# Kernel optimization log

Hardware: AMD Instinct MI355X
Metric: run time of the kernel (lower is better)

The kernel has to match this reference:

```python
import jax, jax.numpy as jnp
from jax import lax
import numpy as np

B, T, H, P = 256, 2048, 256, 24

def setup_inputs() -> dict:
    key = jax.random.key(0)
    ks = jax.random.split(key, 7)
    s_ih = 1.0 / np.sqrt(H)
    return {
        "x": jax.random.normal(ks[0], (B, T, 1), dtype=jnp.float32),
        "W_ih": jax.random.normal(ks[1], (H, 1), dtype=jnp.float32) * s_ih,
        "W_hh": jax.random.normal(ks[2], (H, H), dtype=jnp.float32) * s_ih,
        "b_ih": jax.random.normal(ks[3], (H,), dtype=jnp.float32) * s_ih,
        "b_hh": jax.random.normal(ks[4], (H,), dtype=jnp.float32) * s_ih,
        "W_out": jax.random.normal(ks[5], (P, H), dtype=jnp.float32) * s_ih,
        "b_out": jax.random.normal(ks[6], (P,), dtype=jnp.float32) * s_ih,
    }

def reference(x, W_ih, W_hh, b_ih, b_hh, W_out, b_out):
    # Precompute input projection for all timesteps: [B,T,H]
    xp = jnp.einsum('bti,hi->bth', x, W_ih) + b_ih + b_hh
    h0 = jnp.zeros((x.shape[0], W_hh.shape[0]), dtype=x.dtype)

    def step(h, xt):  # xt: [B,H]
        h_new = jnp.tanh(xt + h @ W_hh.T)
        return h_new, None

    hT, _ = lax.scan(step, h0, xp.transpose(1, 0, 2))  # scan over T
    # Linear head on last hidden state: [B,P]
    return hT @ W_out.T + b_out
```

## Files before the change

### kernel.cpp

```cpp
#include <hip/hip_runtime.h>


#define BB 256
#define TT 2048
#define HH 256
#define PP 24
#define HSTR 20

typedef float v2f __attribute__((ext_vector_type(2)));

struct alignas(16) hquad { v2f lo, hi; };

__device__ __forceinline__ int hidx(int k) { return (k >> 4) * HSTR + (k & 15); }

template<int CTRL>
__device__ __forceinline__ float dppadd(float dst, float src) {
    return dst + __int_as_float(__builtin_amdgcn_update_dpp(
        0, __float_as_int(src), CTRL, 0xf, 0xf, true));
}

__device__ __forceinline__ void lds_barrier() {
    asm volatile("s_waitcnt lgkmcnt(0)\n\ts_barrier" ::: "memory");
}

__global__ __launch_bounds__(512, 1)
void rnn_persist(const float* __restrict__ x,
                 const float* __restrict__ W_ih,
                 const float* __restrict__ W_hh,
                 const float* __restrict__ b_ih,
                 const float* __restrict__ b_hh,
                 const float* __restrict__ W_out,
                 const float* __restrict__ b_out,
                 float* __restrict__ out)
{
    __shared__ __align__(16) float hbuf[2][16 * HSTR];

    const int tid = threadIdx.x;
    const int b   = blockIdx.x;
    const int c   = tid & 15;
    const int g   = tid >> 4;

    hbuf[0][hidx(tid & 255)] = 0.0f;

    const int m[8] = {0, 2, 7, 5, 8, 10, 15, 13};

    v2f w2[8][8];
    #pragma unroll
    for (int s = 0; s < 8; ++s) {
        const int row_idx = 8 * g + ((c ^ m[s]) >> 1);
        const float* row = W_hh + row_idx * HH + 16 * c;
        #pragma unroll
        for (int j = 0; j < 4; ++j) {
            const float4 q = *(const float4*)(row + 4 * j);
            w2[s][2 * j + 0] = (v2f){q.x, q.y};
            w2[s][2 * j + 1] = (v2f){q.z, q.w};
        }
    }

    const int   o_fin = 8 * g + (c >> 1);
    const float wih   = W_ih[o_fin];
    const float cb    = b_ih[o_fin] + b_hh[o_fin];
    const int   widx  = hidx(o_fin);

    __syncthreads();

    const float* hc0 = hbuf[0] + c * HSTR;
    const float* hc1 = hbuf[1] + c * HSTR;
    const float* xb  = x + b * TT;

    auto step = [&](const float* __restrict__ cur, float* __restrict__ nxt,
                    float xt) __attribute__((always_inline)) {
        const hquad* hq = (const hquad*)cur;
        const hquad q0 = hq[0], q1 = hq[1], q2 = hq[2], q3 = hq[3];

        v2f acc[8];
        #pragma unroll
        for (int s = 0; s < 8; ++s) acc[s] = w2[s][0] * q0.lo;
        #pragma unroll
        for (int s = 0; s < 8; ++s)
            acc[s] = __builtin_elementwise_fma(w2[s][1], q0.hi, acc[s]);
        #pragma unroll
        for (int s = 0; s < 8; ++s)
            acc[s] = __builtin_elementwise_fma(w2[s][2], q1.lo, acc[s]);
        #pragma unroll
        for (int s = 0; s < 8; ++s)
            acc[s] = __builtin_elementwise_fma(w2[s][3], q1.hi, acc[s]);
        #pragma unroll
        for (int s = 0; s < 8; ++s)
            acc[s] = __builtin_elementwise_fma(w2[s][4], q2.lo, acc[s]);
        #pragma unroll
        for (int s = 0; s < 8; ++s)
            acc[s] = __builtin_elementwise_fma(w2[s][5], q2.hi, acc[s]);
        #pragma unroll
        for (int s = 0; s < 8; ++s)
            acc[s] = __builtin_elementwise_fma(w2[s][6], q3.lo, acc[s]);
        #pragma unroll
        for (int s = 0; s < 8; ++s)
            acc[s] = __builtin_elementwise_fma(w2[s][7], q3.hi, acc[s]);

        float aa[8];
        #pragma unroll
        for (int s = 0; s < 8; ++s) aa[s] = acc[s].x + acc[s].y;

        float b0 = dppadd<0x128>(aa[0], aa[4]);
        float b1 = dppadd<0x128>(aa[1], aa[5]);
        float b2 = dppadd<0x128>(aa[2], aa[6]);
        float b3 = dppadd<0x128>(aa[3], aa[7]);
        float c0 = dppadd<0x141>(b0, b2);
        float c1 = dppadd<0x141>(b1, b3);
        float d  = dppadd<0x4E>(c0, c1);
        float e  = dppadd<0xB1>(d, d);

        const float u  = fmaf(xt, wih, cb) + e;
        const float p  = __builtin_amdgcn_exp2f(u * 2.8853900817779268f);
        const float th = fmaf(-2.f, __builtin_amdgcn_rcpf(p + 1.f), 1.f);
        nxt[widx] = th;
        lds_barrier();
    };

    float4 xa = *(const float4*)(xb + 0);
    float4 xc = *(const float4*)(xb + 4);
    for (int t = 0; t < TT; t += 8) {
        const int tn = (t + 8 < TT) ? (t + 8) : t;
        const float4 xa_n = *(const float4*)(xb + tn);
        const float4 xc_n = *(const float4*)(xb + tn + 4);
        step(hc0, hbuf[1], xa.x);
        step(hc1, hbuf[0], xa.y);
        step(hc0, hbuf[1], xa.z);
        step(hc1, hbuf[0], xa.w);
        step(hc0, hbuf[1], xc.x);
        step(hc1, hbuf[0], xc.y);
        step(hc0, hbuf[1], xc.z);
        step(hc1, hbuf[0], xc.w);
        xa = xa_n;
        xc = xc_n;
    }

    if (tid < PP) {
        const float* wo = W_out + tid * HH;
        float s0 = 0.f, s1 = 0.f, s2 = 0.f, s3 = 0.f;
        #pragma unroll
        for (int h = 0; h < HH; h += 4) {
            s0 = fmaf(wo[h + 0], hbuf[0][hidx(h + 0)], s0);
            s1 = fmaf(wo[h + 1], hbuf[0][hidx(h + 1)], s1);
            s2 = fmaf(wo[h + 2], hbuf[0][hidx(h + 2)], s2);
            s3 = fmaf(wo[h + 3], hbuf[0][hidx(h + 3)], s3);
        }
        out[b * PP + tid] = b_out[tid] + (s0 + s1) + (s2 + s3);
    }
}

extern "C" void kernel_launch(void* const* d_in, const int* in_sizes, int n_in,
                              void* d_out, int out_size, void* d_ws, size_t ws_size,
                              hipStream_t stream) {
    const float* x     = (const float*)d_in[0];
    const float* W_ih  = (const float*)d_in[1];
    const float* W_hh  = (const float*)d_in[2];
    const float* b_ih  = (const float*)d_in[3];
    const float* b_hh  = (const float*)d_in[4];
    const float* W_out = (const float*)d_in[5];
    const float* b_out = (const float*)d_in[6];
    float* out = (float*)d_out;

    rnn_persist<<<BB, 512, 0, stream>>>(x, W_ih, W_hh, b_ih, b_hh, W_out, b_out, out);
}
```

Measured before the change: 967.8 us.

## Halve block to 256 threads, each computing a full output with 256 weights

Each block now uses 256 threads instead of 512. Every thread owns one hidden unit, holds 256 W_hh weights in registers instead of 128, and does twice the FMAs per step using scalar FMAs rather than packed v2f FMAs. The DPP reduction changes from a fold of pair sums into a 16-way butterfly. This cuts barrier participants and wave count per block. In exchange it doubles per-thread arithmetic and register pressure, with a risk of spilling and of losing packed-FMA throughput.

```diff
diff --git a/kernel.cpp b/kernel.cpp
--- a/kernel.cpp
+++ b/kernel.cpp
@@ -6,10 +6,6 @@
 #define HH 256
 #define PP 24
 #define HSTR 20
-
-typedef float v2f __attribute__((ext_vector_type(2)));
-
-struct alignas(16) hquad { v2f lo, hi; };
 
 __device__ __forceinline__ int hidx(int k) { return (k >> 4) * HSTR + (k & 15); }
 
@@ -23,7 +19,7 @@
     asm volatile("s_waitcnt lgkmcnt(0)\n\ts_barrier" ::: "memory");
 }
 
-__global__ __launch_bounds__(512, 1)
+__global__ __launch_bounds__(256, 1)
 void rnn_persist(const float* __restrict__ x,
                  const float* __restrict__ W_ih,
                  const float* __restrict__ W_hh,
@@ -40,24 +36,24 @@
     const int c   = tid & 15;
     const int g   = tid >> 4;
 
-    hbuf[0][hidx(tid & 255)] = 0.0f;
+    hbuf[0][hidx(tid)] = 0.0f;
 
-    const int m[8] = {0, 2, 7, 5, 8, 10, 15, 13};
+    const int m16[16] = {0,1,2,3, 7,6,5,4, 8,9,10,11, 15,14,13,12};
 
-    v2f w2[8][8];
+    float w[16][16];
     #pragma unroll
-    for (int s = 0; s < 8; ++s) {
-        const int row_idx = 8 * g + ((c ^ m[s]) >> 1);
+    for (int s = 0; s < 16; ++s) {
+        const int row_idx = 16 * g + (c ^ m16[s]);
         const float* row = W_hh + row_idx * HH + 16 * c;
         #pragma unroll
         for (int j = 0; j < 4; ++j) {
-            const float4 q = *(const float4*)(row + 4 * j);
-            w2[s][2 * j + 0] = (v2f){q.x, q.y};
-            w2[s][2 * j + 1] = (v2f){q.z, q.w};
+            const float4 qv = *(const float4*)(row + 4 * j);
+            w[s][4*j+0] = qv.x; w[s][4*j+1] = qv.y;
+            w[s][4*j+2] = qv.z; w[s][4*j+3] = qv.w;
         }
     }
 
-    const int   o_fin = 8 * g + (c >> 1);
+    const int   o_fin = 16 * g + c;
     const float wih   = W_ih[o_fin];
     const float cb    = b_ih[o_fin] + b_hh[o_fin];
     const int   widx  = hidx(o_fin);
@@ -70,46 +66,40 @@
 
     auto step = [&](const float* __restrict__ cur, float* __restrict__ nxt,
                     float xt) __attribute__((always_inline)) {
-        const hquad* hq = (const hquad*)cur;
-        const hquad q0 = hq[0], q1 = hq[1], q2 = hq[2], q3 = hq[3];
+        const float4* hq = (const float4*)cur;
+        const float4 Q0 = hq[0], Q1 = hq[1], Q2 = hq[2], Q3 = hq[3];
+        const float q[16] = {Q0.x,Q0.y,Q0.z,Q0.w, Q1.x,Q1.y,Q1.z,Q1.w,
+                             Q2.x,Q2.y,Q2.z,Q2.w, Q3.x,Q3.y,Q3.z,Q3.w};
 
-        v2f acc[8];
+        float ae[16], ao[16];
         #pragma unroll
-        for (int s = 0; s < 8; ++s) acc[s] = w2[s][0] * q0.lo;
+        for (int s = 0; s < 16; ++s) ae[s] = w[s][0] * q[0];
         #pragma unroll
-        for (int s = 0; s < 8; ++s)
-            acc[s] = __builtin_elementwise_fma(w2[s][1], q0.hi, acc[s]);
+        for (int s = 0; s < 16; ++s) ao[s] = w[s][1] * q[1];
         #pragma unroll
-        for (int s = 0; s < 8; ++s)
-            acc[s] = __builtin_elementwise_fma(w2[s][2], q1.lo, acc[s]);
+        for (int jj = 1; jj < 8; ++jj) {
+            #pragma unroll
+            for (int s = 0; s < 16; ++s)
+                ae[s] = fmaf(w[s][2*jj], q[2*jj], ae[s]);
+            #pragma unroll
+            for (int s = 0; s < 16; ++s)
+                ao[s] = fmaf(w[s][2*jj+1], q[2*jj+1], ao[s]);
+        }
+
+        float aa[16];
         #pragma unroll
-        for (int s = 0; s < 8; ++s)
-            acc[s] = __builtin_elementwise_fma(w2[s][3], q1.hi, acc[s]);
+        for (int s = 0; s < 16; ++s) aa[s] = ae[s] + ao[s];
+
+        float t8[8];
         #pragma unroll
-        for (int s = 0; s < 8; ++s)
-            acc[s] = __builtin_elementwise_fma(w2[s][4], q2.lo, acc[s]);
+        for (int s = 0; s < 8; ++s) t8[s] = dppadd<0x128>(aa[s], aa[s+8]);
+        float t4[4];
         #pragma unroll
-        for (int s = 0; s < 8; ++s)
-            acc[s] = __builtin_elementwise_fma(w2[s][5], q2.hi, acc[s]);
-        #pragma unroll
-        for (int s = 0; s < 8; ++s)
-            acc[s] = __builtin_elementwise_fma(w2[s][6], q3.lo, acc[s]);
-        #pragma unroll
-        for (int s = 0; s < 8; ++s)
-            acc[s] = __builtin_elementwise_fma(w2[s][7], q3.hi, acc[s]);
-
-        float aa[8];
-        #pragma unroll
-        for (int s = 0; s < 8; ++s) aa[s] = acc[s].x + acc[s].y;
-
-        float b0 = dppadd<0x128>(aa[0], aa[4]);
-        float b1 = dppadd<0x128>(aa[1], aa[5]);
-        float b2 = dppadd<0x128>(aa[2], aa[6]);
-        float b3 = dppadd<0x128>(aa[3], aa[7]);
-        float c0 = dppadd<0x141>(b0, b2);
-        float c1 = dppadd<0x141>(b1, b3);
-        float d  = dppadd<0x4E>(c0, c1);
-        float e  = dppadd<0xB1>(d, d);
+        for (int s = 0; s < 4; ++s) t4[s] = dppadd<0x141>(t8[s], t8[s+4]);
+        float t2[2];
+        t2[0] = dppadd<0x4E>(t4[0], t4[2]);
+        t2[1] = dppadd<0x4E>(t4[1], t4[3]);
+        const float e = dppadd<0xB1>(t2[0], t2[1]);
 
         const float u  = fmaf(xt, wih, cb) + e;
         const float p  = __builtin_amdgcn_exp2f(u * 2.8853900817779268f);
@@ -162,5 +152,5 @@
     const float* b_out = (const float*)d_in[6];
     float* out = (float*)d_out;
 
-    rnn_persist<<<BB, 512, 0, stream>>>(x, W_ih, W_hh, b_ih, b_hh, W_out, b_out, out);
+    rnn_persist<<<BB, 256, 0, stream>>>(x, W_ih, W_hh, b_ih, b_hh, W_out, b_out, out);
 }
```

Result: slower. 3.693 ms (+281.6%).

## Store hidden state and recurrent weights in fp16 and use packed dot2

Applied to the files above, without the earlier changes.

Converts the register-resident W_hh slice and the LDS hidden-state buffer to fp16 and replaces packed fp32 FMAs with v_dot2 fp16-to-fp32 accumulation. This halves the instruction count of the per-step matvec and halves LDS read traffic (two 16-byte loads instead of four), and it removes the final pairwise add of accumulator halves. The cost is reduced precision: the hidden state is rounded to fp16 every step across 2048 recurrent steps, which may exceed the accuracy tolerance.

```diff
diff --git a/kernel.cpp b/kernel.cpp
--- a/kernel.cpp
+++ b/kernel.cpp
@@ -5,18 +5,27 @@
 #define TT 2048
 #define HH 256
 #define PP 24
-#define HSTR 20
+#define HSTRH 24
 
-typedef float v2f __attribute__((ext_vector_type(2)));
+typedef _Float16 half_t;
+typedef _Float16 h2 __attribute__((ext_vector_type(2)));
 
-struct alignas(16) hquad { v2f lo, hi; };
+struct alignas(16) hoct { h2 v[4]; };
 
-__device__ __forceinline__ int hidx(int k) { return (k >> 4) * HSTR + (k & 15); }
+__device__ __forceinline__ int hidx16(int k) { return (k >> 4) * HSTRH + (k & 15); }
 
 template<int CTRL>
 __device__ __forceinline__ float dppadd(float dst, float src) {
     return dst + __int_as_float(__builtin_amdgcn_update_dpp(
         0, __float_as_int(src), CTRL, 0xf, 0xf, true));
+}
+
+__device__ __forceinline__ float fdot2f(h2 a, h2 b, float c) {
+#if __has_builtin(__builtin_amdgcn_fdot2)
+    return __builtin_amdgcn_fdot2(a, b, c, false);
+#else
+    return fmaf((float)a.x, (float)b.x, fmaf((float)a.y, (float)b.y, c));
+#endif
 }
 
 __device__ __forceinline__ void lds_barrier() {
@@ -33,79 +42,66 @@
                  const float* __restrict__ b_out,
                  float* __restrict__ out)
 {
-    __shared__ __align__(16) float hbuf[2][16 * HSTR];
+    __shared__ __align__(16) half_t hbuf[2][16 * HSTRH];
 
     const int tid = threadIdx.x;
     const int b   = blockIdx.x;
     const int c   = tid & 15;
     const int g   = tid >> 4;
 
-    hbuf[0][hidx(tid & 255)] = 0.0f;
+    hbuf[0][hidx16(tid & 255)] = (half_t)0.f;
 
     const int m[8] = {0, 2, 7, 5, 8, 10, 15, 13};
 
-    v2f w2[8][8];
+    h2 w2[8][8];
     #pragma unroll
     for (int s = 0; s < 8; ++s) {
         const int row_idx = 8 * g + ((c ^ m[s]) >> 1);
         const float* row = W_hh + row_idx * HH + 16 * c;
         #pragma unroll
-        for (int j = 0; j < 4; ++j) {
-            const float4 q = *(const float4*)(row + 4 * j);
-            w2[s][2 * j + 0] = (v2f){q.x, q.y};
-            w2[s][2 * j + 1] = (v2f){q.z, q.w};
+        for (int j = 0; j < 8; ++j) {
+            w2[s][j] = (h2){(half_t)row[2 * j], (half_t)row[2 * j + 1]};
         }
     }
 
     const int   o_fin = 8 * g + (c >> 1);
     const float wih   = W_ih[o_fin];
     const float cb    = b_ih[o_fin] + b_hh[o_fin];
-    const int   widx  = hidx(o_fin);
+    const int   widx  = hidx16(o_fin);
 
     __syncthreads();
 
-    const float* hc0 = hbuf[0] + c * HSTR;
-    const float* hc1 = hbuf[1] + c * HSTR;
-    const float* xb  = x + b * TT;
+    const half_t* hc0 = hbuf[0] + c * HSTRH;
+    const half_t* hc1 = hbuf[1] + c * HSTRH;
+    const float*  xb  = x + b * TT;
 
-    auto step = [&](const float* __restrict__ cur, float* __restrict__ nxt,
+    auto step = [&](const half_t* __restrict__ cur, half_t* __restrict__ nxt,
                     float xt) __attribute__((always_inline)) {
-        const hquad* hq = (const hquad*)cur;
-        const hquad q0 = hq[0], q1 = hq[1], q2 = hq[2], q3 = hq[3];
+        const hoct* hq = (const hoct*)cur;
+        const hoct qa = hq[0], qb = hq[1];
 
-        v2f acc[8];
+        float acc[8];
         #pragma unroll
-        for (int s = 0; s < 8; ++s) acc[s] = w2[s][0] * q0.lo;
+        for (int s = 0; s < 8; ++s) acc[s] = fdot2f(w2[s][0], qa.v[0], 0.f);
         #pragma unroll
-        for (int s = 0; s < 8; ++s)
-            acc[s] = __builtin_elementwise_fma(w2[s][1], q0.hi, acc[s]);
+        for (int s = 0; s < 8; ++s) acc[s] = fdot2f(w2[s][1], qa.v[1], acc[s]);
         #pragma unroll
-        for (int s = 0; s < 8; ++s)
-            acc[s] = __builtin_elementwise_fma(w2[s][2], q1.lo, acc[s]);
+        for (int s = 0; s < 8; ++s) acc[s] = fdot2f(w2[s][2], qa.v[2], acc[s]);
         #pragma unroll
-        for (int s = 0; s < 8; ++s)
-            acc[s] = __builtin_elementwise_fma(w2[s][3], q1.hi, acc[s]);
+        for (int s = 0; s < 8; ++s) acc[s] = fdot2f(w2[s][3], qa.v[3], acc[s]);
         #pragma unroll
-        for (int s = 0; s < 8; ++s)
-            acc[s] = __builtin_elementwise_fma(w2[s][4], q2.lo, acc[s]);
+        for (int s = 0; s < 8; ++s) acc[s] = fdot2f(w2[s][4], qb.v[0], acc[s]);
         #pragma unroll
-        for (int s = 0; s < 8; ++s)
-            acc[s] = __builtin_elementwise_fma(w2[s][5], q2.hi, acc[s]);
+        for (int s = 0; s < 8; ++s) acc[s] = fdot2f(w2[s][5], qb.v[1], acc[s]);
         #pragma unroll
-        for (int s = 0; s < 8; ++s)
-            acc[s] = __builtin_elementwise_fma(w2[s][6], q3.lo, acc[s]);
+        for (int s = 0; s < 8; ++s) acc[s] = fdot2f(w2[s][6], qb.v[2], acc[s]);
         #pragma unroll
-        for (int s = 0; s < 8; ++s)
-            acc[s] = __builtin_elementwise_fma(w2[s][7], q3.hi, acc[s]);
+        for (int s = 0; s < 8; ++s) acc[s] = fdot2f(w2[s][7], qb.v[3], acc[s]);
 
-        float aa[8];
-        #pragma unroll
-        for (int s = 0; s < 8; ++s) aa[s] = acc[s].x + acc[s].y;
-
-        float b0 = dppadd<0x128>(aa[0], aa[4]);
-        float b1 = dppadd<0x128>(aa[1], aa[5]);
-        float b2 = dppadd<0x128>(aa[2], aa[6]);
-        float b3 = dppadd<0x128>(aa[3], aa[7]);
+        float b0 = dppadd<0x128>(acc[0], acc[4]);
+        float b1 = dppadd<0x128>(acc[1], acc[5]);
+        float b2 = dppadd<0x128>(acc[2], acc[6]);
+        float b3 = dppadd<0x128>(acc[3], acc[7]);
         float c0 = dppadd<0x141>(b0, b2);
         float c1 = dppadd<0x141>(b1, b3);
         float d  = dppadd<0x4E>(c0, c1);
@@ -114,7 +110,7 @@
         const float u  = fmaf(xt, wih, cb) + e;
         const float p  = __builtin_amdgcn_exp2f(u * 2.8853900817779268f);
         const float th = fmaf(-2.f, __builtin_amdgcn_rcpf(p + 1.f), 1.f);
-        nxt[widx] = th;
+        nxt[widx] = (half_t)th;
         lds_barrier();
     };
 
@@ -141,10 +137,10 @@
         float s0 = 0.f, s1 = 0.f, s2 = 0.f, s3 = 0.f;
         #pragma unroll
         for (int h = 0; h < HH; h += 4) {
-            s0 = fmaf(wo[h + 0], hbuf[0][hidx(h + 0)], s0);
-            s1 = fmaf(wo[h + 1], hbuf[0][hidx(h + 1)], s1);
-            s2 = fmaf(wo[h + 2], hbuf[0][hidx(h + 2)], s2);
-            s3 = fmaf(wo[h + 3], hbuf[0][hidx(h + 3)], s3);
+            s0 = fmaf(wo[h + 0], (float)hbuf[0][hidx16(h + 0)], s0);
+            s1 = fmaf(wo[h + 1], (float)hbuf[0][hidx16(h + 1)], s1);
+            s2 = fmaf(wo[h + 2], (float)hbuf[0][hidx16(h + 2)], s2);
+            s3 = fmaf(wo[h + 3], (float)hbuf[0][hidx16(h + 3)], s3);
         }
         out[b * PP + tid] = b_out[tid] + (s0 + s1) + (s2 + s3);
     }
```

After: 893.1 us. 1.08x faster.
